# Kernel tuning notes

Hardware: AMD Instinct MI355X
Metric: run time of the kernel (lower is better)

## Reference

```python
import jax, jax.numpy as jnp
import numpy as np

HID = 1024; HEADS = 16; HD = 64; INTER = 4096; NLAYERS = 4
PATCH = 16; IMG_SIZE = 1024; MAXSIDE = IMG_SIZE // PATCH
THETA = 10000.0; EPS = 1e-5; SCALE = HD ** -0.5


def setup_inputs() -> dict:
    key = jax.random.key(0)
    ks = jax.random.split(key, 11)
    s = 0.02
    w = lambda k, shape: jax.random.normal(k, shape, jnp.float32) * s
    return {
        "img0": jax.random.normal(ks[0], (3, 512, 512), jnp.float32),
        "img1": jax.random.normal(ks[1], (3, 512, 256), jnp.float32),
        "conv_w": w(ks[2], (HID, 3, PATCH, PATCH)),
        "ln_pre_w": jnp.ones((HID,), jnp.float32),
        "attn_norm_w": jnp.ones((NLAYERS, HID), jnp.float32),
        "q_w": w(ks[3], (NLAYERS, HID, HID)),
        "k_w": w(ks[4], (NLAYERS, HID, HID)),
        "v_w": w(ks[5], (NLAYERS, HID, HID)),
        "o_w": w(ks[6], (NLAYERS, HID, HID)),
        "ffn_norm_w": jnp.ones((NLAYERS, HID), jnp.float32),
        "gate_w": w(ks[7], (NLAYERS, INTER, HID)),
        "up_w": w(ks[8], (NLAYERS, INTER, HID)),
        "down_w": w(ks[9], (NLAYERS, HID, INTER)),
    }


def _rms(x, wt):
    return x * jax.lax.rsqrt(jnp.mean(x * x, axis=-1, keepdims=True) + EPS) * wt


def _rot_half(x):
    return jnp.concatenate([-x[..., HD // 2:], x[..., :HD // 2]], axis=-1)


def reference(img0, img1, conv_w, ln_pre_w, attn_norm_w, q_w, k_w, v_w, o_w,
              ffn_norm_w, gate_w, up_w, down_w):
    dn = ('NCHW', 'OIHW', 'NCHW')
    grids, embeds = [], []
    for img in (img0, img1):
        p = jax.lax.conv_general_dilated(img[None], conv_w, (PATCH, PATCH),
                                         'VALID', dimension_numbers=dn)  # [1,HID,h,w]
        h, wd = p.shape[2], p.shape[3]
        grids.append((h, wd))
        embeds.append(p.reshape(1, HID, h * wd).transpose(0, 2, 1))
    x = jnp.concatenate(embeds, axis=1)  # [1, S, HID]
    S = x.shape[1]
    x = _rms(x, ln_pre_w)

    # meshgrid position ids: h*MAXSIDE + w per image
    pids = jnp.concatenate([
        (jnp.arange(h)[:, None] * MAXSIDE + jnp.arange(wd)[None, :]).reshape(-1)
        for h, wd in grids])
    # Pixtral 2D RoPE frequency table
    freqs = 1.0 / THETA ** (jnp.arange(0, HD, 2, dtype=jnp.float32) / HD)  # [HD/2]
    fh = jnp.outer(jnp.arange(MAXSIDE, dtype=jnp.float32), freqs[::2])   # [64, HD/4]
    fw = jnp.outer(jnp.arange(MAXSIDE, dtype=jnp.float32), freqs[1::2])  # [64, HD/4]
    inv = jnp.concatenate([
        jnp.broadcast_to(fh[:, None, :], (MAXSIDE, MAXSIDE, HD // 4)),
        jnp.broadcast_to(fw[None, :, :], (MAXSIDE, MAXSIDE, HD // 4))],
        axis=-1).reshape(-1, HD // 2)
    inv = jnp.concatenate([inv, inv], axis=-1)  # [MAXSIDE^2, HD]
    emb = inv[pids]                              # [S, HD]
    cos = jnp.cos(emb)[None, None]               # [1,1,S,HD]
    sin = jnp.sin(emb)[None, None]

    # block-diagonal additive mask (images don't attend across each other)
    neg = jnp.finfo(jnp.float32).min
    mask = jnp.full((S, S), neg, jnp.float32)
    off = 0
    for h, wd in grids:
        n = h * wd
        mask = mask.at[off:off + n, off:off + n].set(0.0)
        off += n

    def layer(xc, p):
        an, qw, kw, vw, ow, fn, gw, uw, dw = p
        hn = _rms(xc, an)
        heads = lambda y, wm: jnp.einsum('bsd,ed->bse', y, wm).reshape(
            1, S, HEADS, HD).transpose(0, 2, 1, 3)  # [1,H,S,D]
        q, k, v = heads(hn, qw), heads(hn, kw), heads(hn, vw)
        q = q * cos + _rot_half(q) * sin
        k = k * cos + _rot_half(k) * sin
        scores = jnp.einsum('bhqd,bhkd->bhqk', q, k) * SCALE + mask
        aw = jax.nn.softmax(scores.astype(jnp.float32), axis=-1).astype(xc.dtype)
        o = jnp.einsum('bhqk,bhkd->bhqd', aw, v).transpose(0, 2, 1, 3).reshape(1, S, HID)
        h2 = xc + jnp.einsum('bsd,ed->bse', o, ow)
        m = _rms(h2, fn)
        ff = jnp.einsum(
            'bsi,di->bsd',
            jax.nn.silu(jnp.einsum('bsd,id->bsi', m, gw)) * jnp.einsum('bsd,id->bsi', m, uw),
            dw)
        return h2 + ff, None

    out, _ = jax.lax.scan(layer, x, (attn_norm_w, q_w, k_w, v_w, o_w,
                                     ffn_norm_w, gate_w, up_w, down_w))
    return out
```

## Files before the change

kernel.cpp:

```cpp
#include <hip/hip_runtime.h>
#include <hip/hip_bf16.h>
#include <math.h>

#define S_TOT 1536
#define S0    1024
#define HID   1024
#define HEADS 16
#define HD    64
#define INTER 4096
#define NLAYERS 4
#define KCONV 768
#define EPSV  1e-5f
#define SCALEV 0.125f
#define QKVS  3072
#define QKS   2048

typedef __attribute__((ext_vector_type(8))) __bf16 bf16x8;
typedef __attribute__((ext_vector_type(8))) unsigned short u16x8;
typedef __attribute__((ext_vector_type(4))) float f32x4;
typedef __attribute__((address_space(1))) void gvoid;
typedef __attribute__((address_space(3))) void lvoid;

__device__ __forceinline__ ushort f2bf(float f) {
    union { float f; unsigned u; } v; v.f = f;
    unsigned u = v.u;
    return (ushort)((u + 0x7FFFu + ((u >> 16) & 1u)) >> 16);
}
__device__ __forceinline__ float bf2f(ushort b) {
    union { unsigned u; float f; } v; v.u = ((unsigned)b) << 16;
    return v.f;
}

template<int N> __device__ __forceinline__ void wait_vm() {
    if constexpr (N == 0)      asm volatile("s_waitcnt vmcnt(0)" ::: "memory");
    else if constexpr (N == 2) asm volatile("s_waitcnt vmcnt(2)" ::: "memory");
    else if constexpr (N == 4) asm volatile("s_waitcnt vmcnt(4)" ::: "memory");
    else if constexpr (N == 8) asm volatile("s_waitcnt vmcnt(8)" ::: "memory");
    else                       asm volatile("s_waitcnt vmcnt(0)" ::: "memory");
}

__global__ __launch_bounds__(256) void cvt_kernel(
    const float* __restrict__ src, ushort* __restrict__ dst, int n4)
{
    int i = blockIdx.x * 256 + threadIdx.x;
    if (i < n4) {
        float4 v = ((const float4*)src)[i];
        ushort4 o;
        o.x = f2bf(v.x); o.y = f2bf(v.y); o.z = f2bf(v.z); o.w = f2bf(v.w);
        ((ushort4*)dst)[i] = o;
    }
}

__global__ __launch_bounds__(256) void cvt_layer_kernel(
    const float* __restrict__ qw, const float* __restrict__ kw,
    const float* __restrict__ vw, const float* __restrict__ ow,
    const float* __restrict__ gw, const float* __restrict__ uw,
    const float* __restrict__ dw, ushort* __restrict__ dst)
{
    int i = blockIdx.x * 256 + threadIdx.x;
    int e = i << 2;
    const float* src; int off;
    if      (e < (1  << 20)) { src = qw; off = e; }
    else if (e < (2  << 20)) { src = kw; off = e - (1 << 20); }
    else if (e < (3  << 20)) { src = vw; off = e - (2 << 20); }
    else if (e < (4  << 20)) { src = ow; off = e - (3 << 20); }
    else if (e < (8  << 20)) { src = gw; off = e - (4 << 20); }
    else if (e < (12 << 20)) { src = uw; off = e - (8 << 20); }
    else                     { src = dw; off = e - (12 << 20); }
    float4 v = *(const float4*)(src + off);
    ushort4 o;
    o.x = f2bf(v.x); o.y = f2bf(v.y); o.z = f2bf(v.z); o.w = f2bf(v.w);
    *(ushort4*)(dst + e) = o;
}

__global__ __launch_bounds__(256) void im2col_kernel(
    const float* __restrict__ img0, const float* __restrict__ img1,
    ushort* __restrict__ P)
{
    int s = blockIdx.x;
    const float* img; int W, ph, pw;
    if (s < S0) { img = img0; W = 512; ph = s >> 5; pw = s & 31; }
    else { int t = s - S0; img = img1; W = 256; ph = t >> 4; pw = t & 15; }
    for (int k = threadIdx.x; k < KCONV; k += 256) {
        int c = k >> 8; int r = k & 255; int y = r >> 4; int x = r & 15;
        P[(size_t)s * KCONV + k] =
            f2bf(img[(size_t)c * 512 * W + (size_t)(ph * 16 + y) * W + (pw * 16 + x)]);
    }
}

template<int BM, int BN, bool OUT_BF16>
__global__ __launch_bounds__(256) void gemm2p(
    const ushort* __restrict__ A, const ushort* __restrict__ B,
    void* __restrict__ Cout, int M, int N, int K)
{
    constexpr int WMT = BM / 32, WNT = BN / 32;
    constexpr int NLA = (BM * 32) / (8 * 256);
    constexpr int NLB = (BN * 32) / (8 * 256);
    constexpr int NL  = NLA + NLB;
    __shared__ ushort As[2][BM * 32];
    __shared__ ushort Bs[2][BN * 32];
    const int t = threadIdx.x;
    const int bm = blockIdx.x * BM, bn = blockIdx.y * BN;
    const int wave = t >> 6, lane = t & 63;
    const int wm = (wave & 1) * (BM / 2), wn = (wave >> 1) * (BN / 2);
    const int frow = lane & 15, fq = lane >> 4;

    auto stage = [&](int b, int k0) {
        #pragma unroll
        for (int i = 0; i < NLA; ++i) {
            int idx = t + i * 256;
            int r = idx >> 2, c8 = (idx & 3) << 3;
            __builtin_amdgcn_global_load_lds(
                (gvoid*)(A + (size_t)(bm + r) * K + k0 + c8),
                (lvoid*)(&As[b][idx * 8]), 16, 0, 0);
        }
        #pragma unroll
        for (int i = 0; i < NLB; ++i) {
            int idx = t + i * 256;
            int r = idx >> 2, c8 = (idx & 3) << 3;
            __builtin_amdgcn_global_load_lds(
                (gvoid*)(B + (size_t)(bn + r) * K + k0 + c8),
                (lvoid*)(&Bs[b][idx * 8]), 16, 0, 0);
        }
    };

    f32x4 acc[WMT][WNT];
    #pragma unroll
    for (int i = 0; i < WMT; ++i)
        #pragma unroll
        for (int j = 0; j < WNT; ++j) acc[i][j] = (f32x4){0.f, 0.f, 0.f, 0.f};

    stage(0, 0);
    int cur = 0;
    for (int k0 = 0; k0 < K; k0 += 32) {
        const bool more = (k0 + 32) < K;
        if (more) { stage(cur ^ 1, k0 + 32); wait_vm<NL>(); }
        else      { wait_vm<0>(); }
        __builtin_amdgcn_s_barrier();
        __builtin_amdgcn_sched_barrier(0);
        bf16x8 af[WMT], bfr[WNT];
        #pragma unroll
        for (int i = 0; i < WMT; ++i)
            af[i] = *(const bf16x8*)(&As[cur][(wm + 16 * i + frow) * 32 + fq * 8]);
        #pragma unroll
        for (int j = 0; j < WNT; ++j)
            bfr[j] = *(const bf16x8*)(&Bs[cur][(wn + 16 * j + frow) * 32 + fq * 8]);
        asm volatile("s_waitcnt lgkmcnt(0)" ::: "memory");
        __builtin_amdgcn_sched_barrier(0);
        __builtin_amdgcn_s_barrier();
        #pragma unroll
        for (int i = 0; i < WMT; ++i)
            #pragma unroll
            for (int j = 0; j < WNT; ++j)
                acc[i][j] = __builtin_amdgcn_mfma_f32_16x16x32_bf16(
                    af[i], bfr[j], acc[i][j], 0, 0, 0);
        cur ^= 1;
    }
    #pragma unroll
    for (int i = 0; i < WMT; ++i) {
        #pragma unroll
        for (int j = 0; j < WNT; ++j) {
            #pragma unroll
            for (int r = 0; r < 4; ++r) {
                int row = bm + wm + 16 * i + fq * 4 + r;
                int col = bn + wn + 16 * j + frow;
                float vv = acc[i][j][r];
                if (OUT_BF16) ((ushort*)Cout)[(size_t)row * N + col] = f2bf(vv);
                else          ((float*)Cout)[(size_t)row * N + col] = vv;
            }
        }
    }
}

template<int SPLITK>
__global__ __launch_bounds__(256) void gemm2p_sk(
    const ushort* __restrict__ A, const ushort* __restrict__ B,
    float* __restrict__ P, int M, int N, int K)
{
    constexpr int BM = 128, BN = 128;
    constexpr int NL = 4;
    __shared__ ushort As[2][BM * 32];
    __shared__ ushort Bs[2][BN * 32];
    const int t = threadIdx.x;
    const int bm = blockIdx.x * BM, bn = blockIdx.y * BN;
    const int kc = K / SPLITK;
    const int kb = blockIdx.z * kc, ke = kb + kc;
    const int wave = t >> 6, lane = t & 63;
    const int wm = (wave & 1) * 64, wn = (wave >> 1) * 64;
    const int frow = lane & 15, fq = lane >> 4;

    auto stage = [&](int b, int k0) {
        #pragma unroll
        for (int i = 0; i < 2; ++i) {
            int idx = t + i * 256;
            int r = idx >> 2, c8 = (idx & 3) << 3;
            __builtin_amdgcn_global_load_lds(
                (gvoid*)(A + (size_t)(bm + r) * K + k0 + c8),
                (lvoid*)(&As[b][idx * 8]), 16, 0, 0);
        }
        #pragma unroll
        for (int i = 0; i < 2; ++i) {
            int idx = t + i * 256;
            int r = idx >> 2, c8 = (idx & 3) << 3;
            __builtin_amdgcn_global_load_lds(
                (gvoid*)(B + (size_t)(bn + r) * K + k0 + c8),
                (lvoid*)(&Bs[b][idx * 8]), 16, 0, 0);
        }
    };

    f32x4 acc[4][4];
    #pragma unroll
    for (int i = 0; i < 4; ++i)
        #pragma unroll
        for (int j = 0; j < 4; ++j) acc[i][j] = (f32x4){0.f, 0.f, 0.f, 0.f};

    stage(0, kb);
    int cur = 0;
    for (int k0 = kb; k0 < ke; k0 += 32) {
        const bool more = (k0 + 32) < ke;
        if (more) { stage(cur ^ 1, k0 + 32); wait_vm<NL>(); }
        else      { wait_vm<0>(); }
        __builtin_amdgcn_s_barrier();
        __builtin_amdgcn_sched_barrier(0);
        bf16x8 af[4], bfr[4];
        #pragma unroll
        for (int i = 0; i < 4; ++i)
            af[i] = *(const bf16x8*)(&As[cur][(wm + 16 * i + frow) * 32 + fq * 8]);
        #pragma unroll
        for (int j = 0; j < 4; ++j)
            bfr[j] = *(const bf16x8*)(&Bs[cur][(wn + 16 * j + frow) * 32 + fq * 8]);
        asm volatile("s_waitcnt lgkmcnt(0)" ::: "memory");
        __builtin_amdgcn_sched_barrier(0);
        __builtin_amdgcn_s_barrier();
        #pragma unroll
        for (int i = 0; i < 4; ++i)
            #pragma unroll
            for (int j = 0; j < 4; ++j)
                acc[i][j] = __builtin_amdgcn_mfma_f32_16x16x32_bf16(
                    af[i], bfr[j], acc[i][j], 0, 0, 0);
        cur ^= 1;
    }
    float* Pz = P + (size_t)blockIdx.z * M * N;
    #pragma unroll
    for (int i = 0; i < 4; ++i) {
        #pragma unroll
        for (int j = 0; j < 4; ++j) {
            #pragma unroll
            for (int r = 0; r < 4; ++r) {
                int row = bm + wm + 16 * i + fq * 4 + r;
                int col = bn + wn + 16 * j + frow;
                Pz[(size_t)row * N + col] = acc[i][j][r];
            }
        }
    }
}

__global__ __launch_bounds__(256) void reduce4_kernel(
    const float* __restrict__ P, float* __restrict__ x, int n4)
{
    int i = blockIdx.x * 256 + threadIdx.x;
    if (i >= n4) return;
    const int n = n4 << 2;
    float4 a  = ((const float4*)x)[i];
    float4 p0 = ((const float4*)P)[i];
    float4 p1 = ((const float4*)(P + (size_t)n))[i];
    float4 p2 = ((const float4*)(P + (size_t)2 * n))[i];
    float4 p3 = ((const float4*)(P + (size_t)3 * n))[i];
    a.x += p0.x + p1.x + p2.x + p3.x;
    a.y += p0.y + p1.y + p2.y + p3.y;
    a.z += p0.z + p1.z + p2.z + p3.z;
    a.w += p0.w + p1.w + p2.w + p3.w;
    ((float4*)x)[i] = a;
}

__global__ __launch_bounds__(256) void rms_kernel(
    const float* __restrict__ in, const float* __restrict__ w,
    float* __restrict__ out)
{
    int row = blockIdx.x;
    const float* xr = in + (size_t)row * HID;
    float ss = 0.f;
    for (int i = threadIdx.x; i < HID; i += 256) { float v = xr[i]; ss += v * v; }
    #pragma unroll
    for (int off = 32; off > 0; off >>= 1) ss += __shfl_down(ss, off, 64);
    __shared__ float red[4];
    int wid = threadIdx.x >> 6;
    if ((threadIdx.x & 63) == 0) red[wid] = ss;
    __syncthreads();
    if (threadIdx.x == 0)
        red[0] = rsqrtf((red[0] + red[1] + red[2] + red[3]) / HID + EPSV);
    __syncthreads();
    float rs = red[0];
    for (int i = threadIdx.x; i < HID; i += 256)
        out[(size_t)row * HID + i] = xr[i] * rs * w[i];
}

__global__ __launch_bounds__(256) void rms_bf_kernel(
    const float* __restrict__ in, const float* __restrict__ w,
    ushort* __restrict__ out)
{
    int row = blockIdx.x;
    const float* xr = in + (size_t)row * HID;
    float ss = 0.f;
    for (int i = threadIdx.x; i < HID; i += 256) { float v = xr[i]; ss += v * v; }
    #pragma unroll
    for (int off = 32; off > 0; off >>= 1) ss += __shfl_down(ss, off, 64);
    __shared__ float red[4];
    int wid = threadIdx.x >> 6;
    if ((threadIdx.x & 63) == 0) red[wid] = ss;
    __syncthreads();
    if (threadIdx.x == 0)
        red[0] = rsqrtf((red[0] + red[1] + red[2] + red[3]) / HID + EPSV);
    __syncthreads();
    float rs = red[0];
    for (int i = threadIdx.x; i < HID; i += 256)
        out[(size_t)row * HID + i] = f2bf(xr[i] * rs * w[i]);
}

__global__ void rope_tab_kernel(float* __restrict__ cs, float* __restrict__ sn)
{
    int s = blockIdx.x; int j = threadIdx.x;
    int h, w;
    if (s < S0) { h = s >> 5; w = s & 31; }
    else { int t = s - S0; h = t >> 4; w = t & 15; }
    float f;
    if (j < 16) f = (float)h * powf(10000.f, -(4.f * j) / 64.f);
    else        f = (float)w * powf(10000.f, -(4.f * (j - 16) + 2.f) / 64.f);
    cs[s * 32 + j] = cosf(f);
    sn[s * 32 + j] = sinf(f);
}

__global__ __launch_bounds__(256) void rope_bf_kernel(
    const float* __restrict__ qkv, ushort* __restrict__ qkb,
    const float* __restrict__ cs, const float* __restrict__ sn)
{
    int idx = blockIdx.x * 256 + threadIdx.x;
    int s = idx >> 11, c = idx & 2047;
    int part = c >> 10, cc = c & 1023;
    int hh = cc >> 6, d = cc & 63, j = d & 31;
    size_t base = (size_t)s * QKVS + part * 1024 + hh * HD;
    float xa = qkv[base + j], xb = qkv[base + 32 + j];
    float cv = cs[s * 32 + j], sv = sn[s * 32 + j];
    float out = (d < 32) ? (xa * cv - xb * sv) : (xb * cv + xa * sv);
    qkb[idx] = f2bf(out);
}

__global__ __launch_bounds__(256) void vtrans_kernel(
    const float* __restrict__ qkv, ushort* __restrict__ vT)
{
    __shared__ float T[64][65];
    int st = blockIdx.x;
    int hh = blockIdx.y;
    int s0 = st << 6;
    int t = threadIdx.x;
    #pragma unroll
    for (int i = 0; i < 16; i += 4) {
        int u = t + ((i >> 2) << 8);
        int r = u >> 4, c4 = (u & 15) << 2;
        float4 v = *(const float4*)(qkv + (size_t)(s0 + r) * QKVS + 2048 + hh * HD + c4);
        T[r][c4 + 0] = v.x; T[r][c4 + 1] = v.y; T[r][c4 + 2] = v.z; T[r][c4 + 3] = v.w;
    }
    __syncthreads();
    int d = t >> 2, sg = (t & 3) << 4;
    ushort buf[16];
    #pragma unroll
    for (int j = 0; j < 16; ++j) buf[j] = f2bf(T[sg + j][d]);
    ushort* dst = vT + ((size_t)hh * HD + d) * S_TOT + s0 + sg;
    *(u16x8*)dst = *(u16x8*)buf;
    *(u16x8*)(dst + 8) = *(u16x8*)(buf + 8);
}

__global__ __launch_bounds__(256) void flash_mfma_kernel(
    const ushort* __restrict__ qkb, const ushort* __restrict__ vT,
    ushort* __restrict__ o)
{
    __shared__ ushort Ks[64 * 72];
    __shared__ ushort Vt[64 * 72];
    __shared__ ushort Ps[4 * 16 * 72];
    int tile = blockIdx.x;
    int hh = blockIdx.y;
    int segStart, q0, nkt;
    if (tile < 16) { segStart = 0; q0 = tile << 6; nkt = 16; }
    else { segStart = S0; q0 = S0 + ((tile - 16) << 6); nkt = 8; }
    const int t = threadIdx.x;
    const int wave = t >> 6, lane = t & 63;
    const int c = lane & 15, fq = lane >> 4;
    const int wq = wave << 4;
    ushort* Pw = Ps + wave * 16 * 72;

    bf16x8 qf[2];
    #pragma unroll
    for (int ks = 0; ks < 2; ++ks)
        qf[ks] = *(const bf16x8*)(qkb + (size_t)(q0 + wq + c) * QKS + hh * HD + ks * 32 + fq * 8);

    float m_i[4], l_i[4];
    f32x4 accO[4];
    #pragma unroll
    for (int r = 0; r < 4; ++r) { m_i[r] = -1e30f; l_i[r] = 0.f; }
    #pragma unroll
    for (int nt = 0; nt < 4; ++nt) accO[nt] = (f32x4){0.f, 0.f, 0.f, 0.f};

    for (int kt = 0; kt < nkt; ++kt) {
        int kbase = segStart + (kt << 6);
        __syncthreads();
        #pragma unroll
        for (int i = 0; i < 2; ++i) {
            int u = t + (i << 8);
            int r = u >> 3, c8 = (u & 7) << 3;
            u16x8 kv = *(const u16x8*)(qkb + (size_t)(kbase + r) * QKS + 1024 + hh * HD + c8);
            *(u16x8*)(Ks + r * 72 + c8) = kv;
            u16x8 vv = *(const u16x8*)(vT + ((size_t)hh * HD + r) * S_TOT + kbase + c8);
            *(u16x8*)(Vt + r * 72 + c8) = vv;
        }
        __syncthreads();

        f32x4 acc[4];
        #pragma unroll
        for (int nt = 0; nt < 4; ++nt) acc[nt] = (f32x4){0.f, 0.f, 0.f, 0.f};
        #pragma unroll
        for (int ks = 0; ks < 2; ++ks) {
            #pragma unroll
            for (int nt = 0; nt < 4; ++nt) {
                bf16x8 bfr = *(const bf16x8*)(Ks + (nt * 16 + c) * 72 + ks * 32 + fq * 8);
                acc[nt] = __builtin_amdgcn_mfma_f32_16x16x32_bf16(qf[ks], bfr, acc[nt], 0, 0, 0);
            }
        }

        #pragma unroll
        for (int r = 0; r < 4; ++r) {
            float s0v = acc[0][r] * SCALEV, s1v = acc[1][r] * SCALEV;
            float s2v = acc[2][r] * SCALEV, s3v = acc[3][r] * SCALEV;
            float rm = fmaxf(fmaxf(s0v, s1v), fmaxf(s2v, s3v));
            #pragma unroll
            for (int msk = 1; msk < 16; msk <<= 1)
                rm = fmaxf(rm, __shfl_xor(rm, msk, 64));
            float mn = fmaxf(m_i[r], rm);
            float al = __expf(m_i[r] - mn);
            float p0 = __expf(s0v - mn), p1 = __expf(s1v - mn);
            float p2 = __expf(s2v - mn), p3 = __expf(s3v - mn);
            float rs = p0 + p1 + p2 + p3;
            #pragma unroll
            for (int msk = 1; msk < 16; msk <<= 1)
                rs += __shfl_xor(rs, msk, 64);
            l_i[r] = l_i[r] * al + rs;
            m_i[r] = mn;
            #pragma unroll
            for (int nt = 0; nt < 4; ++nt) accO[nt][r] *= al;
            int qrow = (fq << 2) + r;
            Pw[qrow * 72 + 0  + c] = f2bf(p0);
            Pw[qrow * 72 + 16 + c] = f2bf(p1);
            Pw[qrow * 72 + 32 + c] = f2bf(p2);
            Pw[qrow * 72 + 48 + c] = f2bf(p3);
        }

        #pragma unroll
        for (int ks = 0; ks < 2; ++ks) {
            bf16x8 pa = *(const bf16x8*)(Pw + c * 72 + ks * 32 + fq * 8);
            #pragma unroll
            for (int nt = 0; nt < 4; ++nt) {
                bf16x8 bv = *(const bf16x8*)(Vt + (nt * 16 + c) * 72 + ks * 32 + fq * 8);
                accO[nt] = __builtin_amdgcn_mfma_f32_16x16x32_bf16(pa, bv, accO[nt], 0, 0, 0);
            }
        }
    }

    #pragma unroll
    for (int r = 0; r < 4; ++r) {
        float inv = 1.f / l_i[r];
        int row = q0 + wq + (fq << 2) + r;
        #pragma unroll
        for (int nt = 0; nt < 4; ++nt)
            o[(size_t)row * HID + hh * HD + nt * 16 + c] = f2bf(accO[nt][r] * inv);
    }
}

__global__ __launch_bounds__(256) void silu_mul_bf_kernel(
    const ushort* __restrict__ gu, ushort* __restrict__ gb)
{
    int i = blockIdx.x * 256 + threadIdx.x;
    int s = i >> 12, cc = i & 4095;
    float x = bf2f(gu[(size_t)s * 8192 + cc]);
    float u = bf2f(gu[(size_t)s * 8192 + 4096 + cc]);
    float sg = 1.f / (1.f + __expf(-x));
    gb[i] = f2bf(x * sg * u);
}

__global__ __launch_bounds__(256) void copy_kernel(
    const float* __restrict__ src, float* __restrict__ dst, int n)
{
    int i = blockIdx.x * 256 + threadIdx.x;
    if (i < n) dst[i] = src[i];
}

extern "C" void kernel_launch(void* const* d_in, const int* in_sizes, int n_in,
                              void* d_out, int out_size, void* d_ws, size_t ws_size,
                              hipStream_t stream)
{
    const float* img0        = (const float*)d_in[0];
    const float* img1        = (const float*)d_in[1];
    const float* conv_w      = (const float*)d_in[2];
    const float* ln_pre_w    = (const float*)d_in[3];
    const float* attn_norm_w = (const float*)d_in[4];
    const float* q_w         = (const float*)d_in[5];
    const float* k_w         = (const float*)d_in[6];
    const float* v_w         = (const float*)d_in[7];
    const float* o_w         = (const float*)d_in[8];
    const float* ffn_norm_w  = (const float*)d_in[9];
    const float* gate_w      = (const float*)d_in[10];
    const float* up_w        = (const float*)d_in[11];
    const float* down_w      = (const float*)d_in[12];

    char* p = (char*)d_ws;
    float* x    = (float*)p;   p += (size_t)1572864 * 4;
    float* qkv  = (float*)p;   p += (size_t)4718592 * 4;
    float* cs   = (float*)p;   p += (size_t)49152 * 4;
    float* sn   = (float*)p;   p += (size_t)49152 * 4;
    ushort* qkb = (ushort*)p;  p += (size_t)3145728 * 2;
    ushort* vTb = (ushort*)p;  p += (size_t)1572864 * 2;
    ushort* hnb = (ushort*)p;  p += (size_t)1572864 * 2;
    ushort* obb = (ushort*)p;  p += (size_t)1572864 * 2;
    ushort* gub = (ushort*)p;  p += (size_t)12582912 * 2;
    ushort* gb  = (ushort*)p;  p += (size_t)6291456 * 2;
    ushort* Pb  = (ushort*)p;  p += (size_t)1179648 * 2;
    ushort* cvb = (ushort*)p;  p += (size_t)786432 * 2;
    ushort* wbuf= (ushort*)p;  p += (size_t)16777216 * 2;

    ushort* wqkv = wbuf;
    ushort* wo   = wbuf + 3145728;
    ushort* wgu  = wbuf + 4194304;
    ushort* wdn  = wbuf + 12582912;

    float* skP = (float*)gub;

    dim3 blk(256);

    cvt_kernel<<<768, blk, 0, stream>>>(conv_w, cvb, 786432 / 4);
    im2col_kernel<<<S_TOT, blk, 0, stream>>>(img0, img1, Pb);
    gemm2p<64, 64, false><<<dim3(24, 16), blk, 0, stream>>>(
        Pb, cvb, x, S_TOT, HID, KCONV);
    rms_kernel<<<S_TOT, blk, 0, stream>>>(x, ln_pre_w, x);
    rope_tab_kernel<<<S_TOT, 32, 0, stream>>>(cs, sn);

    for (int l = 0; l < NLAYERS; ++l) {
        cvt_layer_kernel<<<16384, blk, 0, stream>>>(
            q_w + (size_t)l * 1048576, k_w + (size_t)l * 1048576,
            v_w + (size_t)l * 1048576, o_w + (size_t)l * 1048576,
            gate_w + (size_t)l * 4194304, up_w + (size_t)l * 4194304,
            down_w + (size_t)l * 4194304, wbuf);

        rms_bf_kernel<<<S_TOT, blk, 0, stream>>>(x, attn_norm_w + (size_t)l * HID, hnb);
        gemm2p<128, 128, false><<<dim3(12, 24), blk, 0, stream>>>(
            hnb, wqkv, qkv, S_TOT, QKVS, HID);
        rope_bf_kernel<<<(S_TOT * QKS) / 256, blk, 0, stream>>>(qkv, qkb, cs, sn);
        vtrans_kernel<<<dim3(24, HEADS), blk, 0, stream>>>(qkv, vTb);
        flash_mfma_kernel<<<dim3(24, HEADS), blk, 0, stream>>>(qkb, vTb, obb);
        gemm2p_sk<4><<<dim3(12, 8, 4), blk, 0, stream>>>(
            obb, wo, skP, S_TOT, HID, HID);
        reduce4_kernel<<<1536, blk, 0, stream>>>(skP, x, S_TOT * HID / 4);
        rms_bf_kernel<<<S_TOT, blk, 0, stream>>>(x, ffn_norm_w + (size_t)l * HID, hnb);
        gemm2p<128, 128, true><<<dim3(12, 64), blk, 0, stream>>>(
            hnb, wgu, gub, S_TOT, 2 * INTER, HID);
        silu_mul_bf_kernel<<<(S_TOT * INTER) / 256, blk, 0, stream>>>(gub, gb);
        gemm2p_sk<4><<<dim3(12, 8, 4), blk, 0, stream>>>(
            gb, wdn, skP, S_TOT, HID, INTER);
        reduce4_kernel<<<1536, blk, 0, stream>>>(skP, x, S_TOT * HID / 4);
    }
    copy_kernel<<<(S_TOT * HID) / 256, blk, 0, stream>>>(x, (float*)d_out, S_TOT * HID);
}
```

Before: 0.9997 ms.

## Fuse RoPE into QKV GEMM epilogue and SiLU-mul into gate/up GEMM

The QKV GEMM now applies RoPE in its epilogue and writes bf16 q/k plus bf16 V directly. This removes the fp32 qkv buffer and the separate rope kernel, and the V transpose now reads bf16. The gate/up weights are interleaved in 16-row chunks during conversion, so each GEMM tile holds matching gate and up columns and can compute silu(g)*u in the epilogue. This drops the intermediate gub buffer and the silu kernel, cutting global memory traffic and launches. In exchange the epilogue does scattered 2-byte stores, and correctness depends on the interleaved weight layout matching the epilogue's column mapping.

```diff
diff --git a/kernel.cpp b/kernel.cpp
--- a/kernel.cpp
+++ b/kernel.cpp
@@ -12,7 +12,6 @@
 #define KCONV 768
 #define EPSV  1e-5f
 #define SCALEV 0.125f
-#define QKVS  3072
 #define QKS   2048
 
 typedef __attribute__((ext_vector_type(8))) __bf16 bf16x8;
@@ -59,18 +58,26 @@
 {
     int i = blockIdx.x * 256 + threadIdx.x;
     int e = i << 2;
-    const float* src; int off;
-    if      (e < (1  << 20)) { src = qw; off = e; }
-    else if (e < (2  << 20)) { src = kw; off = e - (1 << 20); }
-    else if (e < (3  << 20)) { src = vw; off = e - (2 << 20); }
-    else if (e < (4  << 20)) { src = ow; off = e - (3 << 20); }
-    else if (e < (8  << 20)) { src = gw; off = e - (4 << 20); }
-    else if (e < (12 << 20)) { src = uw; off = e - (8 << 20); }
-    else                     { src = dw; off = e - (12 << 20); }
+    const float* src; int off; size_t de;
+    if      (e < (1  << 20)) { src = qw; off = e;             de = e; }
+    else if (e < (2  << 20)) { src = kw; off = e - (1 << 20); de = e; }
+    else if (e < (3  << 20)) { src = vw; off = e - (2 << 20); de = e; }
+    else if (e < (4  << 20)) { src = ow; off = e - (3 << 20); de = e; }
+    else if (e < (8  << 20)) {
+        src = gw; off = e - (4 << 20);
+        int chan = off >> 10, col = off & 1023;
+        de = (size_t)(4 << 20) + (size_t)(((chan >> 4) << 5) + (chan & 15)) * 1024 + col;
+    }
+    else if (e < (12 << 20)) {
+        src = uw; off = e - (8 << 20);
+        int chan = off >> 10, col = off & 1023;
+        de = (size_t)(4 << 20) + (size_t)(((chan >> 4) << 5) + 16 + (chan & 15)) * 1024 + col;
+    }
+    else                     { src = dw; off = e - (12 << 20); de = e; }
     float4 v = *(const float4*)(src + off);
     ushort4 o;
     o.x = f2bf(v.x); o.y = f2bf(v.y); o.z = f2bf(v.z); o.w = f2bf(v.w);
-    *(ushort4*)(dst + e) = o;
+    *(ushort4*)(dst + de) = o;
 }
 
 __global__ __launch_bounds__(256) void im2col_kernel(
@@ -87,6 +94,26 @@
             f2bf(img[(size_t)c * 512 * W + (size_t)(ph * 16 + y) * W + (pw * 16 + x)]);
     }
 }
+
+#define GEMM2P_CORE(BM_, BN_, NLA_, NLB_)                                        \
+    auto stage = [&](int b, int k0) {                                            \
+        _Pragma("unroll")                                                        \
+        for (int i_ = 0; i_ < NLA_; ++i_) {                                      \
+            int idx = t + i_ * 256;                                              \
+            int r_ = idx >> 2, c8_ = (idx & 3) << 3;                             \
+            __builtin_amdgcn_global_load_lds(                                    \
+                (gvoid*)(A + (size_t)(bm + r_) * K + k0 + c8_),                  \
+                (lvoid*)(&As[b][idx * 8]), 16, 0, 0);                            \
+        }                                                                        \
+        _Pragma("unroll")                                                        \
+        for (int i_ = 0; i_ < NLB_; ++i_) {                                      \
+            int idx = t + i_ * 256;                                              \
+            int r_ = idx >> 2, c8_ = (idx & 3) << 3;                             \
+            __builtin_amdgcn_global_load_lds(                                    \
+                (gvoid*)(B + (size_t)(bn + r_) * K + k0 + c8_),                  \
+                (lvoid*)(&Bs[b][idx * 8]), 16, 0, 0);                            \
+        }                                                                        \
+    };
 
 template<int BM, int BN, bool OUT_BF16>
 __global__ __launch_bounds__(256) void gemm2p(
@@ -104,25 +131,7 @@
     const int wave = t >> 6, lane = t & 63;
     const int wm = (wave & 1) * (BM / 2), wn = (wave >> 1) * (BN / 2);
     const int frow = lane & 15, fq = lane >> 4;
-
-    auto stage = [&](int b, int k0) {
-        #pragma unroll
-        for (int i = 0; i < NLA; ++i) {
-            int idx = t + i * 256;
-            int r = idx >> 2, c8 = (idx & 3) << 3;
-            __builtin_amdgcn_global_load_lds(
-                (gvoid*)(A + (size_t)(bm + r) * K + k0 + c8),
-                (lvoid*)(&As[b][idx * 8]), 16, 0, 0);
-        }
-        #pragma unroll
-        for (int i = 0; i < NLB; ++i) {
-            int idx = t + i * 256;
-            int r = idx >> 2, c8 = (idx & 3) << 3;
-            __builtin_amdgcn_global_load_lds(
-                (gvoid*)(B + (size_t)(bn + r) * K + k0 + c8),
-                (lvoid*)(&Bs[b][idx * 8]), 16, 0, 0);
-        }
-    };
+    GEMM2P_CORE(BM, BN, NLA, NLB)
 
     f32x4 acc[WMT][WNT];
     #pragma unroll
@@ -172,13 +181,154 @@
     }
 }
 
+__global__ __launch_bounds__(256) void gemm2p_qkv(
+    const ushort* __restrict__ A, const ushort* __restrict__ B,
+    ushort* __restrict__ qkb, ushort* __restrict__ vb,
+    const float* __restrict__ cs, const float* __restrict__ sn, int K)
+{
+    constexpr int BM = 128, BN = 128;
+    __shared__ ushort As[2][BM * 32];
+    __shared__ ushort Bs[2][BN * 32];
+    const int t = threadIdx.x;
+    const int bm = blockIdx.x * BM, bn = blockIdx.y * BN;
+    const int wave = t >> 6, lane = t & 63;
+    const int wm = (wave & 1) * 64, wn = (wave >> 1) * 64;
+    const int frow = lane & 15, fq = lane >> 4;
+    GEMM2P_CORE(BM, BN, 2, 2)
+
+    f32x4 acc[4][4];
+    #pragma unroll
+    for (int i = 0; i < 4; ++i)
+        #pragma unroll
+        for (int j = 0; j < 4; ++j) acc[i][j] = (f32x4){0.f, 0.f, 0.f, 0.f};
+
+    stage(0, 0);
+    int cur = 0;
+    for (int k0 = 0; k0 < K; k0 += 32) {
+        const bool more = (k0 + 32) < K;
+        if (more) { stage(cur ^ 1, k0 + 32); wait_vm<4>(); }
+        else      { wait_vm<0>(); }
+        __builtin_amdgcn_s_barrier();
+        __builtin_amdgcn_sched_barrier(0);
+        bf16x8 af[4], bfr[4];
+        #pragma unroll
+        for (int i = 0; i < 4; ++i)
+            af[i] = *(const bf16x8*)(&As[cur][(wm + 16 * i + frow) * 32 + fq * 8]);
+        #pragma unroll
+        for (int j = 0; j < 4; ++j)
+            bfr[j] = *(const bf16x8*)(&Bs[cur][(wn + 16 * j + frow) * 32 + fq * 8]);
+        asm volatile("s_waitcnt lgkmcnt(0)" ::: "memory");
+        __builtin_amdgcn_sched_barrier(0);
+        __builtin_amdgcn_s_barrier();
+        #pragma unroll
+        for (int i = 0; i < 4; ++i)
+            #pragma unroll
+            for (int j = 0; j < 4; ++j)
+                acc[i][j] = __builtin_amdgcn_mfma_f32_16x16x32_bf16(
+                    af[i], bfr[j], acc[i][j], 0, 0, 0);
+        cur ^= 1;
+    }
+    const int colbase = bn + wn;
+    const int part = colbase >> 10;
+    if (part < 2) {
+        #pragma unroll
+        for (int i = 0; i < 4; ++i) {
+            #pragma unroll
+            for (int r = 0; r < 4; ++r) {
+                int row = bm + wm + 16 * i + fq * 4 + r;
+                float cv0 = cs[row * 32 + frow],      sv0 = sn[row * 32 + frow];
+                float cv1 = cs[row * 32 + 16 + frow], sv1 = sn[row * 32 + 16 + frow];
+                float xa0 = acc[i][0][r], xa1 = acc[i][1][r];
+                float xb0 = acc[i][2][r], xb1 = acc[i][3][r];
+                ushort* dst = qkb + (size_t)row * QKS + (part << 10) + (colbase & 1023) + frow;
+                dst[0]  = f2bf(xa0 * cv0 - xb0 * sv0);
+                dst[16] = f2bf(xa1 * cv1 - xb1 * sv1);
+                dst[32] = f2bf(xb0 * cv0 + xa0 * sv0);
+                dst[48] = f2bf(xb1 * cv1 + xa1 * sv1);
+            }
+        }
+    } else {
+        #pragma unroll
+        for (int i = 0; i < 4; ++i)
+            #pragma unroll
+            for (int j = 0; j < 4; ++j)
+                #pragma unroll
+                for (int r = 0; r < 4; ++r) {
+                    int row = bm + wm + 16 * i + fq * 4 + r;
+                    vb[(size_t)row * 1024 + (colbase & 1023) + 16 * j + frow] =
+                        f2bf(acc[i][j][r]);
+                }
+    }
+}
+
+__global__ __launch_bounds__(256) void gemm2p_gu(
+    const ushort* __restrict__ A, const ushort* __restrict__ B,
+    ushort* __restrict__ gb, int K)
+{
+    constexpr int BM = 128, BN = 128;
+    __shared__ ushort As[2][BM * 32];
+    __shared__ ushort Bs[2][BN * 32];
+    const int t = threadIdx.x;
+    const int bm = blockIdx.x * BM, bn = blockIdx.y * BN;
+    const int wave = t >> 6, lane = t & 63;
+    const int wm = (wave & 1) * 64, wn = (wave >> 1) * 64;
+    const int frow = lane & 15, fq = lane >> 4;
+    GEMM2P_CORE(BM, BN, 2, 2)
+
+    f32x4 acc[4][4];
+    #pragma unroll
+    for (int i = 0; i < 4; ++i)
+        #pragma unroll
+        for (int j = 0; j < 4; ++j) acc[i][j] = (f32x4){0.f, 0.f, 0.f, 0.f};
+
+    stage(0, 0);
+    int cur = 0;
+    for (int k0 = 0; k0 < K; k0 += 32) {
+        const bool more = (k0 + 32) < K;
+        if (more) { stage(cur ^ 1, k0 + 32); wait_vm<4>(); }
+        else      { wait_vm<0>(); }
+        __builtin_amdgcn_s_barrier();
+        __builtin_amdgcn_sched_barrier(0);
+        bf16x8 af[4], bfr[4];
+        #pragma unroll
+        for (int i = 0; i < 4; ++i)
+            af[i] = *(const bf16x8*)(&As[cur][(wm + 16 * i + frow) * 32 + fq * 8]);
+        #pragma unroll
+        for (int j = 0; j < 4; ++j)
+            bfr[j] = *(const bf16x8*)(&Bs[cur][(wn + 16 * j + frow) * 32 + fq * 8]);
+        asm volatile("s_waitcnt lgkmcnt(0)" ::: "memory");
+        __builtin_amdgcn_sched_barrier(0);
+        __builtin_amdgcn_s_barrier();
+        #pragma unroll
+        for (int i = 0; i < 4; ++i)
+            #pragma unroll
+            for (int j = 0; j < 4; ++j)
+                acc[i][j] = __builtin_amdgcn_mfma_f32_16x16x32_bf16(
+                    af[i], bfr[j], acc[i][j], 0, 0, 0);
+        cur ^= 1;
+    }
+    #pragma unroll
+    for (int i = 0; i < 4; ++i) {
+        #pragma unroll
+        for (int jp = 0; jp < 2; ++jp) {
+            int chan = ((bn + wn) >> 1) + jp * 16 + frow;
+            #pragma unroll
+            for (int r = 0; r < 4; ++r) {
+                int row = bm + wm + 16 * i + fq * 4 + r;
+                float g = acc[i][2 * jp][r], u = acc[i][2 * jp + 1][r];
+                float sg = 1.f / (1.f + __expf(-g));
+                gb[(size_t)row * INTER + chan] = f2bf(g * sg * u);
+            }
+        }
+    }
+}
+
 template<int SPLITK>
 __global__ __launch_bounds__(256) void gemm2p_sk(
     const ushort* __restrict__ A, const ushort* __restrict__ B,
     float* __restrict__ P, int M, int N, int K)
 {
     constexpr int BM = 128, BN = 128;
-    constexpr int NL = 4;
     __shared__ ushort As[2][BM * 32];
     __shared__ ushort Bs[2][BN * 32];
     const int t = threadIdx.x;
@@ -188,25 +338,7 @@
     const int wave = t >> 6, lane = t & 63;
     const int wm = (wave & 1) * 64, wn = (wave >> 1) * 64;
     const int frow = lane & 15, fq = lane >> 4;
-
-    auto stage = [&](int b, int k0) {
-        #pragma unroll
-        for (int i = 0; i < 2; ++i) {
-            int idx = t + i * 256;
-            int r = idx >> 2, c8 = (idx & 3) << 3;
-            __builtin_amdgcn_global_load_lds(
-                (gvoid*)(A + (size_t)(bm + r) * K + k0 + c8),
-                (lvoid*)(&As[b][idx * 8]), 16, 0, 0);
-        }
-        #pragma unroll
-        for (int i = 0; i < 2; ++i) {
-            int idx = t + i * 256;
-            int r = idx >> 2, c8 = (idx & 3) << 3;
-            __builtin_amdgcn_global_load_lds(
-                (gvoid*)(B + (size_t)(bn + r) * K + k0 + c8),
-                (lvoid*)(&Bs[b][idx * 8]), 16, 0, 0);
-        }
-    };
+    GEMM2P_CORE(BM, BN, 2, 2)
 
     f32x4 acc[4][4];
     #pragma unroll
@@ -218,7 +350,7 @@
     int cur = 0;
     for (int k0 = kb; k0 < ke; k0 += 32) {
         const bool more = (k0 + 32) < ke;
-        if (more) { stage(cur ^ 1, k0 + 32); wait_vm<NL>(); }
+        if (more) { stage(cur ^ 1, k0 + 32); wait_vm<4>(); }
         else      { wait_vm<0>(); }
         __builtin_amdgcn_s_barrier();
         __builtin_amdgcn_sched_barrier(0);
@@ -330,41 +462,26 @@
     sn[s * 32 + j] = sinf(f);
 }
 
-__global__ __launch_bounds__(256) void rope_bf_kernel(
-    const float* __restrict__ qkv, ushort* __restrict__ qkb,
-    const float* __restrict__ cs, const float* __restrict__ sn)
-{
-    int idx = blockIdx.x * 256 + threadIdx.x;
-    int s = idx >> 11, c = idx & 2047;
-    int part = c >> 10, cc = c & 1023;
-    int hh = cc >> 6, d = cc & 63, j = d & 31;
-    size_t base = (size_t)s * QKVS + part * 1024 + hh * HD;
-    float xa = qkv[base + j], xb = qkv[base + 32 + j];
-    float cv = cs[s * 32 + j], sv = sn[s * 32 + j];
-    float out = (d < 32) ? (xa * cv - xb * sv) : (xb * cv + xa * sv);
-    qkb[idx] = f2bf(out);
-}
-
-__global__ __launch_bounds__(256) void vtrans_kernel(
-    const float* __restrict__ qkv, ushort* __restrict__ vT)
-{
-    __shared__ float T[64][65];
+__global__ __launch_bounds__(256) void vtrans_bf_kernel(
+    const ushort* __restrict__ vb, ushort* __restrict__ vT)
+{
+    __shared__ ushort T[64][72];
     int st = blockIdx.x;
     int hh = blockIdx.y;
     int s0 = st << 6;
     int t = threadIdx.x;
     #pragma unroll
-    for (int i = 0; i < 16; i += 4) {
-        int u = t + ((i >> 2) << 8);
-        int r = u >> 4, c4 = (u & 15) << 2;
-        float4 v = *(const float4*)(qkv + (size_t)(s0 + r) * QKVS + 2048 + hh * HD + c4);
-        T[r][c4 + 0] = v.x; T[r][c4 + 1] = v.y; T[r][c4 + 2] = v.z; T[r][c4 + 3] = v.w;
+    for (int i = 0; i < 2; ++i) {
+        int u = t + (i << 8);
+        int r = u >> 3, c8 = (u & 7) << 3;
+        u16x8 v = *(const u16x8*)(vb + (size_t)(s0 + r) * 1024 + hh * HD + c8);
+        *(u16x8*)(&T[r][c8]) = v;
     }
     __syncthreads();
     int d = t >> 2, sg = (t & 3) << 4;
     ushort buf[16];
     #pragma unroll
-    for (int j = 0; j < 16; ++j) buf[j] = f2bf(T[sg + j][d]);
+    for (int j = 0; j < 16; ++j) buf[j] = T[sg + j][d];
     ushort* dst = vT + ((size_t)hh * HD + d) * S_TOT + s0 + sg;
     *(u16x8*)dst = *(u16x8*)buf;
     *(u16x8*)(dst + 8) = *(u16x8*)(buf + 8);
@@ -474,17 +591,6 @@
     }
 }
 
-__global__ __launch_bounds__(256) void silu_mul_bf_kernel(
-    const ushort* __restrict__ gu, ushort* __restrict__ gb)
-{
-    int i = blockIdx.x * 256 + threadIdx.x;
-    int s = i >> 12, cc = i & 4095;
-    float x = bf2f(gu[(size_t)s * 8192 + cc]);
-    float u = bf2f(gu[(size_t)s * 8192 + 4096 + cc]);
-    float sg = 1.f / (1.f + __expf(-x));
-    gb[i] = f2bf(x * sg * u);
-}
-
 __global__ __launch_bounds__(256) void copy_kernel(
     const float* __restrict__ src, float* __restrict__ dst, int n)
 {
@@ -512,15 +618,15 @@
 
     char* p = (char*)d_ws;
     float* x    = (float*)p;   p += (size_t)1572864 * 4;
-    float* qkv  = (float*)p;   p += (size_t)4718592 * 4;
     float* cs   = (float*)p;   p += (size_t)49152 * 4;
     float* sn   = (float*)p;   p += (size_t)49152 * 4;
     ushort* qkb = (ushort*)p;  p += (size_t)3145728 * 2;
+    ushort* vb  = (ushort*)p;  p += (size_t)1572864 * 2;
     ushort* vTb = (ushort*)p;  p += (size_t)1572864 * 2;
     ushort* hnb = (ushort*)p;  p += (size_t)1572864 * 2;
     ushort* obb = (ushort*)p;  p += (size_t)1572864 * 2;
-    ushort* gub = (ushort*)p;  p += (size_t)12582912 * 2;
     ushort* gb  = (ushort*)p;  p += (size_t)6291456 * 2;
+    float* skP  = (float*)p;   p += (size_t)6291456 * 4;
     ushort* Pb  = (ushort*)p;  p += (size_t)1179648 * 2;
     ushort* cvb = (ushort*)p;  p += (size_t)786432 * 2;
     ushort* wbuf= (ushort*)p;  p += (size_t)16777216 * 2;
@@ -529,8 +635,6 @@
     ushort* wo   = wbuf + 3145728;
     ushort* wgu  = wbuf + 4194304;
     ushort* wdn  = wbuf + 12582912;
-
-    float* skP = (float*)gub;
 
     dim3 blk(256);
 
@@ -549,18 +653,15 @@
             down_w + (size_t)l * 4194304, wbuf);
 
         rms_bf_kernel<<<S_TOT, blk, 0, stream>>>(x, attn_norm_w + (size_t)l * HID, hnb);
-        gemm2p<128, 128, false><<<dim3(12, 24), blk, 0, stream>>>(
-            hnb, wqkv, qkv, S_TOT, QKVS, HID);
-        rope_bf_kernel<<<(S_TOT * QKS) / 256, blk, 0, stream>>>(qkv, qkb, cs, sn);
-        vtrans_kernel<<<dim3(24, HEADS), blk, 0, stream>>>(qkv, vTb);
+        gemm2p_qkv<<<dim3(12, 24), blk, 0, stream>>>(
+            hnb, wqkv, qkb, vb, cs, sn, HID);
+        vtrans_bf_kernel<<<dim3(24, HEADS), blk, 0, stream>>>(vb, vTb);
         flash_mfma_kernel<<<dim3(24, HEADS), blk, 0, stream>>>(qkb, vTb, obb);
         gemm2p_sk<4><<<dim3(12, 8, 4), blk, 0, stream>>>(
             obb, wo, skP, S_TOT, HID, HID);
         reduce4_kernel<<<1536, blk, 0, stream>>>(skP, x, S_TOT * HID / 4);
         rms_bf_kernel<<<S_TOT, blk, 0, stream>>>(x, ffn_norm_w + (size_t)l * HID, hnb);
-        gemm2p<128, 128, true><<<dim3(12, 64), blk, 0, stream>>>(
-            hnb, wgu, gub, S_TOT, 2 * INTER, HID);
-        silu_mul_bf_kernel<<<(S_TOT * INTER) / 256, blk, 0, stream>>>(gub, gb);
+        gemm2p_gu<<<dim3(12, 64), blk, 0, stream>>>(hnb, wgu, gb, HID);
         gemm2p_sk<4><<<dim3(12, 8, 4), blk, 0, stream>>>(
             gb, wdn, skP, S_TOT, HID, INTER);
         reduce4_kernel<<<1536, blk, 0, stream>>>(skP, x, S_TOT * HID / 4);
```

After: 927.9 us. 7.2% less time.
